# Kernel tuning notes

Measured on AMD Instinct MI355X. Metric: run time of the kernel, lower is better.

## Reference

```python
import jax, jax.numpy as jnp
import numpy as np

DIM = 1024
N_HEADS = 16
HEAD_DIM = DIM // N_HEADS
LN_EPS = 1e-5


def layer_norm(x, gamma, beta, eps=LN_EPS):
    mu = jnp.mean(x, axis=-1, keepdims=True)
    var = jnp.var(x, axis=-1, keepdims=True)
    return (x - mu) * jax.lax.rsqrt(var + eps) * gamma + beta


def setup_inputs() -> dict:
    key = jax.random.key(0)
    ks = jax.random.split(key, 12)
    B, Nq, Nc, D = 2, 1024, 4096, DIM
    s = 1.0 / np.sqrt(D)  # torch Linear default init scale (uniform bound)
    inp = {
        "query": jax.random.normal(ks[0], (B, Nq, D), jnp.float32),
        "context": jax.random.normal(ks[1], (B, Nc, D), jnp.float32),
        "wq": jax.random.uniform(ks[2], (D, D), jnp.float32, -s, s),
        "bq": jax.random.uniform(ks[3], (D,), jnp.float32, -s, s),
        "wk": jax.random.uniform(ks[4], (D, D), jnp.float32, -s, s),
        "bk": jax.random.uniform(ks[5], (D,), jnp.float32, -s, s),
        "wv": jax.random.uniform(ks[6], (D, D), jnp.float32, -s, s),
        "bv": jax.random.uniform(ks[7], (D,), jnp.float32, -s, s),
        "wo": jax.random.uniform(ks[8], (D, D), jnp.float32, -s, s),
        "bo": jax.random.uniform(ks[9], (D,), jnp.float32, -s, s),
        "g_q": jnp.ones((D,), jnp.float32),
        "b_q": jnp.zeros((D,), jnp.float32),
        "g_kv": jnp.ones((D,), jnp.float32),
        "b_kv": jnp.zeros((D,), jnp.float32),
    }
    return inp


def reference(query, context, wq, bq, wk, bk, wv, bv, wo, bo, g_q, b_q, g_kv, b_kv):
    B, Nq, D = query.shape
    Nc = context.shape[1]
    H, Hd = N_HEADS, HEAD_DIM

    qn = layer_norm(query, g_q, b_q)        # [B,Nq,D]
    cn = layer_norm(context, g_kv, b_kv)    # [B,Nc,D]

    # torch Linear: y = x @ W.T + b; weights here stored as [out,in]
    Q = (jnp.einsum('bnd,ed->bne', qn, wq) + bq).reshape(B, Nq, H, Hd)
    K = (jnp.einsum('bnd,ed->bne', cn, wk) + bk).reshape(B, Nc, H, Hd)
    V = (jnp.einsum('bnd,ed->bne', cn, wv) + bv).reshape(B, Nc, H, Hd)

    scale = 1.0 / np.sqrt(Hd)
    scores = jnp.einsum('bqhd,bkhd->bhqk', Q, K) * scale  # [B,H,Nq,Nc]
    attn = jax.nn.softmax(scores, axis=-1)
    out = jnp.einsum('bhqk,bkhd->bqhd', attn, V).reshape(B, Nq, D)

    return qn + (jnp.einsum('bnd,ed->bne', out, wo) + bo)
```

## Files before the change

kernel.cpp:

```cpp
#include <hip/hip_runtime.h>

typedef unsigned short u16;
typedef __attribute__((ext_vector_type(8))) __bf16 bf16x8;
typedef __attribute__((ext_vector_type(4))) float f32x4;

struct alignas(8) U16x4 { u16 x, y, z, w; };

#define MFMA16(a, b, c) __builtin_amdgcn_mfma_f32_16x16x32_bf16(a, b, c, 0, 0, 0)

__device__ __forceinline__ u16 f2bf(float f) {
    union { float f; unsigned u; } v; v.f = f;
    unsigned r = v.u + 0x7fffu + ((v.u >> 16) & 1u);
    return (u16)(r >> 16);
}

__device__ __forceinline__ unsigned cvt_pk_bf16(float lo, float hi) {
    unsigned r;
    asm("v_cvt_pk_bf16_f32 %0, %1, %2" : "=v"(r) : "v"(lo), "v"(hi));
    return r;
}

__device__ __forceinline__ float fexp2(float x) {
    float r;
    asm("v_exp_f32 %0, %1" : "=v"(r) : "v"(x));
    return r;
}

__device__ __forceinline__ void gload_lds16(const void* g, void* l) {
    __builtin_amdgcn_global_load_lds(
        (__attribute__((address_space(1))) void*)g,
        (__attribute__((address_space(3))) void*)l, 16, 0, 0);
}

__global__ __launch_bounds__(256)
void prep(const float* __restrict__ query, const float* __restrict__ context,
          const float* __restrict__ g_q, const float* __restrict__ b_q,
          const float* __restrict__ g_kv, const float* __restrict__ b_kv,
          float* __restrict__ qn32, u16* __restrict__ qnb, u16* __restrict__ cnb,
          const float4* __restrict__ w0, const float4* __restrict__ w1,
          const float4* __restrict__ w2, const float4* __restrict__ w3,
          U16x4* __restrict__ o0, U16x4* __restrict__ o1,
          U16x4* __restrict__ o2, U16x4* __restrict__ o3)
{
    const int blk = blockIdx.x;
    if (blk < 2560) {
        const float *x, *g, *be; float* y32; u16* y16; int rb;
        if (blk < 512) { x = query;   g = g_q;  be = b_q;  y32 = qn32;    y16 = qnb; rb = blk; }
        else           { x = context; g = g_kv; be = b_kv; y32 = nullptr; y16 = cnb; rb = blk - 512; }
        const int wid = threadIdx.x >> 6, lane = threadIdx.x & 63;
        const size_t row = (size_t)rb * 4 + wid;
        const float4* xr = (const float4*)(x + row * 1024);
        float4 v[4];
        float s = 0.f, ss = 0.f;
#pragma unroll
        for (int i = 0; i < 4; ++i) {
            v[i] = xr[i * 64 + lane];
            s  += (v[i].x + v[i].y) + (v[i].z + v[i].w);
            ss += (v[i].x * v[i].x + v[i].y * v[i].y) + (v[i].z * v[i].z + v[i].w * v[i].w);
        }
#pragma unroll
        for (int o = 32; o; o >>= 1) { s += __shfl_xor(s, o, 64); ss += __shfl_xor(ss, o, 64); }
        const float mu = s * (1.f / 1024.f);
        const float rstd = rsqrtf(ss * (1.f / 1024.f) - mu * mu + 1e-5f);
#pragma unroll
        for (int i = 0; i < 4; ++i) {
            float4 gv = ((const float4*)g)[i * 64 + lane];
            float4 bv = ((const float4*)be)[i * 64 + lane];
            float4 o;
            o.x = (v[i].x - mu) * rstd * gv.x + bv.x;
            o.y = (v[i].y - mu) * rstd * gv.y + bv.y;
            o.z = (v[i].z - mu) * rstd * gv.z + bv.z;
            o.w = (v[i].w - mu) * rstd * gv.w + bv.w;
            if (y32) ((float4*)(y32 + row * 1024))[i * 64 + lane] = o;
            U16x4 pk = { f2bf(o.x), f2bf(o.y), f2bf(o.z), f2bf(o.w) };
            ((U16x4*)(y16 + row * 1024))[i * 64 + lane] = pk;
        }
    } else {
        const int i = (blk - 2560) * 256 + threadIdx.x;
        float4 v;
        v = w0[i]; o0[i] = { f2bf(v.x), f2bf(v.y), f2bf(v.z), f2bf(v.w) };
        v = w1[i]; o1[i] = { f2bf(v.x), f2bf(v.y), f2bf(v.z), f2bf(v.w) };
        v = w2[i]; o2[i] = { f2bf(v.x), f2bf(v.y), f2bf(v.z), f2bf(v.w) };
        v = w3[i]; o3[i] = { f2bf(v.x), f2bf(v.y), f2bf(v.z), f2bf(v.w) };
    }
}

__global__ __launch_bounds__(512, 4)
void gemm_kv(const u16* __restrict__ A, const u16* __restrict__ Wk,
             const u16* __restrict__ Wv, const float* __restrict__ bkp,
             const float* __restrict__ bvp, u16* __restrict__ Kout,
             u16* __restrict__ Vt)
{
    constexpr int K = 1024, N = 1024, BK = 64;
    __shared__ __align__(16) u16 sA[128 * BK];
    __shared__ __align__(16) u16 sK[128 * BK];
    __shared__ __align__(16) u16 sV[128 * BK];
    const int tid = threadIdx.x, wid = tid >> 6, lane = tid & 63;
    const int lr = lane & 15, lg = lane >> 4;
    const int wr = wid >> 2, wc = wid & 3;
    const int row0 = blockIdx.x * 128, col0 = blockIdx.y * 128;
    const int srow = wid * 8 + (lane >> 3), scol = (lane & 7) * 8;

    const u16* Ag = A  + (size_t)(row0 + srow) * K + scol;
    const u16* Kg = Wk + (size_t)(col0 + srow) * K + scol;
    const u16* Vg = Wv + (size_t)(col0 + srow) * K + scol;

    f32x4 ka[4][2], va[4][2];
#pragma unroll
    for (int m = 0; m < 4; ++m)
#pragma unroll
        for (int n = 0; n < 2; ++n) {
            ka[m][n] = (f32x4){0.f, 0.f, 0.f, 0.f};
            va[m][n] = (f32x4){0.f, 0.f, 0.f, 0.f};
        }

    for (int k0 = 0; k0 < K; k0 += BK) {
        __syncthreads();
#pragma unroll
        for (int i = 0; i < 2; ++i) {
            gload_lds16(Ag + (size_t)i * 64 * K + k0, (char*)sA + i * 8192 + wid * 1024);
            gload_lds16(Kg + (size_t)i * 64 * K + k0, (char*)sK + i * 8192 + wid * 1024);
            gload_lds16(Vg + (size_t)i * 64 * K + k0, (char*)sV + i * 8192 + wid * 1024);
        }
        __syncthreads();
#pragma unroll
        for (int kk = 0; kk < 2; ++kk) {
            bf16x8 af[4], bk[2], bv[2];
#pragma unroll
            for (int m = 0; m < 4; ++m)
                af[m] = *(const bf16x8*)&sA[(wr * 64 + m * 16 + lr) * BK + kk * 32 + lg * 8];
#pragma unroll
            for (int n = 0; n < 2; ++n) {
                bk[n] = *(const bf16x8*)&sK[(wc * 32 + n * 16 + lr) * BK + kk * 32 + lg * 8];
                bv[n] = *(const bf16x8*)&sV[(wc * 32 + n * 16 + lr) * BK + kk * 32 + lg * 8];
            }
#pragma unroll
            for (int m = 0; m < 4; ++m)
#pragma unroll
                for (int n = 0; n < 2; ++n) {
                    ka[m][n] = MFMA16(af[m], bk[n], ka[m][n]);
                    va[m][n] = MFMA16(af[m], bv[n], va[m][n]);
                }
        }
    }

#pragma unroll
    for (int m = 0; m < 4; ++m) {
#pragma unroll
        for (int n = 0; n < 2; ++n) {
            const int r = row0 + wr * 64 + m * 16 + lg * 4;
            const int c = col0 + wc * 32 + n * 16 + lr;
            const float kb = bkp[c], vb = bvp[c];
#pragma unroll
            for (int j = 0; j < 4; ++j)
                Kout[(size_t)(r + j) * N + c] = f2bf(ka[m][n][j] + kb);
            const size_t base = ((size_t)(r >> 12) * 1024 + c) * 4096 + (r & 4095);
            U16x4 pk = { f2bf(va[m][n][0] + vb), f2bf(va[m][n][1] + vb),
                         f2bf(va[m][n][2] + vb), f2bf(va[m][n][3] + vb) };
            *(U16x4*)&Vt[base] = pk;
        }
    }
}

template<int MODE>
__global__ __launch_bounds__(256)
void gemm_bt64(const u16* __restrict__ A, const u16* __restrict__ W,
               const float* __restrict__ bias, const float* __restrict__ resid,
               void* __restrict__ Cp, int M, int N, int K, float alpha)
{
    constexpr int BK = 64;
    __shared__ __align__(16) u16 sA[64 * BK];
    __shared__ __align__(16) u16 sB[128 * BK];
    const int tid = threadIdx.x, wid = tid >> 6, lane = tid & 63;
    const int lr = lane & 15, lg = lane >> 4;
    const int wr = wid >> 1, wc = wid & 1;
    const int row0 = blockIdx.x * 64, col0 = blockIdx.y * 128;
    const int srow = wid * 8 + (lane >> 3), scol = (lane & 7) * 8;

    const u16* Ag = A + (size_t)(row0 + srow) * K + scol;
    const u16* Wg = W + (size_t)(col0 + srow) * K + scol;

    f32x4 acc[2][4];
#pragma unroll
    for (int m = 0; m < 2; ++m)
#pragma unroll
        for (int n = 0; n < 4; ++n) acc[m][n] = (f32x4){0.f, 0.f, 0.f, 0.f};

    for (int k0 = 0; k0 < K; k0 += BK) {
        __syncthreads();
#pragma unroll
        for (int i = 0; i < 2; ++i)
            gload_lds16(Ag + (size_t)i * 32 * K + k0, (char*)sA + i * 4096 + wid * 1024);
#pragma unroll
        for (int i = 0; i < 4; ++i)
            gload_lds16(Wg + (size_t)i * 32 * K + k0, (char*)sB + i * 4096 + wid * 1024);
        __syncthreads();
#pragma unroll
        for (int kk = 0; kk < 2; ++kk) {
            bf16x8 af[2], bfr[4];
#pragma unroll
            for (int m = 0; m < 2; ++m)
                af[m] = *(const bf16x8*)&sA[(wr * 32 + m * 16 + lr) * BK + kk * 32 + lg * 8];
#pragma unroll
            for (int n = 0; n < 4; ++n)
                bfr[n] = *(const bf16x8*)&sB[(wc * 64 + n * 16 + lr) * BK + kk * 32 + lg * 8];
#pragma unroll
            for (int m = 0; m < 2; ++m)
#pragma unroll
                for (int n = 0; n < 4; ++n)
                    acc[m][n] = MFMA16(af[m], bfr[n], acc[m][n]);
        }
    }

#pragma unroll
    for (int m = 0; m < 2; ++m) {
#pragma unroll
        for (int n = 0; n < 4; ++n) {
            const int r = row0 + wr * 32 + m * 16 + lg * 4;
            const int c = col0 + wc * 64 + n * 16 + lr;
            const float bv = bias[c];
            if constexpr (MODE == 0) {
                u16* C = (u16*)Cp;
#pragma unroll
                for (int j = 0; j < 4; ++j)
                    C[(size_t)(r + j) * N + c] = f2bf((acc[m][n][j] + bv) * alpha);
            } else {
                float* C = (float*)Cp;
#pragma unroll
                for (int j = 0; j < 4; ++j)
                    C[(size_t)(r + j) * N + c] =
                        (acc[m][n][j] + bv) * alpha + resid[(size_t)(r + j) * N + c];
            }
        }
    }
}

__global__ __launch_bounds__(512, 4)
void attn_fwd(const u16* __restrict__ Q, const u16* __restrict__ Kg,
              const u16* __restrict__ Vt, u16* __restrict__ O)
{
    constexpr int D = 1024, CSTR = 19;
    __shared__ __align__(16) char smem[81920];

    const int tid = threadIdx.x, wid = tid >> 6, lane = tid & 63;
    const int grp = wid >> 2, w = wid & 3;
    const int lr = lane & 15, lg = lane >> 4;
    const int rs = lr & 7;
    const int pkey = (lr & 7) << 4;

    const int fid = blockIdx.x;
    const int wkid = (fid & 7) * 64 + (fid >> 3);
    const int qblk = wkid & 15, h = (wkid >> 4) & 15, b = wkid >> 8;
    const int q0 = qblk * 64 + w * 16;

    const u16* Qrow = Q + (size_t)(b * 1024 + q0 + lr) * D + h * 64;
    const bf16x8 qf0 = *(const bf16x8*)(Qrow + lg * 8);
    const bf16x8 qf1 = *(const bf16x8*)(Qrow + 32 + lg * 8);

    const int srow = w * 8 + (lane >> 3);
    const int scol = ((lane & 7) ^ (srow & 7)) * 8;
    const u16* kp = Kg + (size_t)(b * 4096 + grp * 2048 + srow) * D + h * 64 + scol;
    const u16* vp = Vt + ((size_t)(b * 16 + h) * 64 + srow) * 4096 + grp * 2048 + scol;

    char* sProw = smem + 65536 + wid * 2048 + lr * 128;

    f32x4 po[4];
#pragma unroll
    for (int df = 0; df < 4; ++df) po[df] = (f32x4){0.f, 0.f, 0.f, 0.f};
    float m = -INFINITY, l = 0.f;
    bf16x8 vr0, vr1, vr2, vr3, vr4, vr5, vr6, vr7;

    auto pv_step = [&]() {
        bf16x8 pf0 = *(const bf16x8*)(sProw + ((lg * 16) ^ pkey));
        bf16x8 pf1 = *(const bf16x8*)(sProw + ((64 + lg * 16) ^ pkey));
        po[0] = MFMA16(vr0, pf0, po[0]);
        po[1] = MFMA16(vr1, pf0, po[1]);
        po[2] = MFMA16(vr2, pf0, po[2]);
        po[3] = MFMA16(vr3, pf0, po[3]);
        po[0] = MFMA16(vr4, pf1, po[0]);
        po[1] = MFMA16(vr5, pf1, po[1]);
        po[2] = MFMA16(vr6, pf1, po[2]);
        po[3] = MFMA16(vr7, pf1, po[3]);
    };

    {
        char* kd = smem + grp * 8192 + w * 1024;
        char* vd = smem + 32768 + grp * 8192 + w * 1024;
        gload_lds16(kp,                      kd);
        gload_lds16(kp + (size_t)32 * D,     kd + 4096);
        gload_lds16(vp,                      vd);
        gload_lds16(vp + (size_t)32 * 4096,  vd + 4096);
        kp += (size_t)64 * D; vp += 64;
    }
    asm volatile("s_waitcnt vmcnt(0)" ::: "memory");
    asm volatile("s_barrier" ::: "memory");

    for (int t = 0; t < 32; ++t) {
        const int cur = t & 1;
        if (t < 31) {
            char* kd = smem + (cur ^ 1) * 16384 + grp * 8192 + w * 1024;
            char* vd = smem + 32768 + (cur ^ 1) * 16384 + grp * 8192 + w * 1024;
            gload_lds16(kp,                      kd);
            gload_lds16(kp + (size_t)32 * D,     kd + 4096);
            gload_lds16(vp,                      vd);
            gload_lds16(vp + (size_t)32 * 4096,  vd + 4096);
            kp += (size_t)64 * D; vp += 64;
        }

        const u16* kb = (const u16*)(smem + cur * 16384 + grp * 8192);
        const u16* vb = (const u16*)(smem + 32768 + cur * 16384 + grp * 8192);

        __builtin_amdgcn_s_setprio(1);
        if (t > 0) pv_step();

        f32x4 s4[4];
#pragma unroll
        for (int f = 0; f < 4; ++f) {
            const int r = f * 16 + lr;
            bf16x8 k0v = *(const bf16x8*)&kb[r * 64 + (lg ^ rs) * 8];
            bf16x8 k1v = *(const bf16x8*)&kb[r * 64 + ((lg + 4) ^ rs) * 8];
            f32x4 z = (f32x4){0.f, 0.f, 0.f, 0.f};
            z = MFMA16(k0v, qf0, z);
            s4[f] = MFMA16(k1v, qf1, z);
        }
        __builtin_amdgcn_s_setprio(0);

        vr0 = *(const bf16x8*)&vb[(0 * 16 + lr) * 64 + ((0 + lg) ^ rs) * 8];
        vr1 = *(const bf16x8*)&vb[(1 * 16 + lr) * 64 + ((0 + lg) ^ rs) * 8];
        vr2 = *(const bf16x8*)&vb[(2 * 16 + lr) * 64 + ((0 + lg) ^ rs) * 8];
        vr3 = *(const bf16x8*)&vb[(3 * 16 + lr) * 64 + ((0 + lg) ^ rs) * 8];
        vr4 = *(const bf16x8*)&vb[(0 * 16 + lr) * 64 + ((4 + lg) ^ rs) * 8];
        vr5 = *(const bf16x8*)&vb[(1 * 16 + lr) * 64 + ((4 + lg) ^ rs) * 8];
        vr6 = *(const bf16x8*)&vb[(2 * 16 + lr) * 64 + ((4 + lg) ^ rs) * 8];
        vr7 = *(const bf16x8*)&vb[(3 * 16 + lr) * 64 + ((4 + lg) ^ rs) * 8];

        float pmax = fmaxf(fmaxf(fmaxf(s4[0][0], s4[0][1]), fmaxf(s4[0][2], s4[0][3])),
                     fmaxf(fmaxf(fmaxf(s4[1][0], s4[1][1]), fmaxf(s4[1][2], s4[1][3])),
                     fmaxf(fmaxf(fmaxf(s4[2][0], s4[2][1]), fmaxf(s4[2][2], s4[2][3])),
                           fmaxf(fmaxf(s4[3][0], s4[3][1]), fmaxf(s4[3][2], s4[3][3])))));
        if (!__all(pmax <= m)) {
            float tmax = fmaxf(pmax, __shfl_xor(pmax, 16, 64));
            tmax = fmaxf(tmax, __shfl_xor(tmax, 32, 64));
            const float mn = fmaxf(m, tmax);
            const float corr = fexp2(m - mn);
            l *= corr;
#pragma unroll
            for (int df = 0; df < 4; ++df) po[df] *= corr;
            m = mn;
        }
        float lsum = 0.f;
        uint2 pk[4];
#pragma unroll
        for (int f = 0; f < 4; ++f) {
            float p0 = fexp2(s4[f][0] - m);
            float p1 = fexp2(s4[f][1] - m);
            float p2 = fexp2(s4[f][2] - m);
            float p3 = fexp2(s4[f][3] - m);
            lsum += (p0 + p1) + (p2 + p3);
            pk[f].x = cvt_pk_bf16(p0, p1);
            pk[f].y = cvt_pk_bf16(p2, p3);
        }
        l += lsum;

#pragma unroll
        for (int f = 0; f < 4; ++f)
            *(uint2*)(sProw + ((f * 32 + lg * 8) ^ pkey)) = pk[f];

        asm volatile("s_waitcnt vmcnt(0) lgkmcnt(0)" ::: "memory");
        asm volatile("s_barrier" ::: "memory");
    }

    pv_step();

    l += __shfl_xor(l, 16, 64);
    l += __shfl_xor(l, 32, 64);

    float* cb = (float*)smem;
    if (grp == 1) {
        float* dst = cb + (size_t)(w * 64 + lane) * CSTR;
        dst[0] = m; dst[1] = l;
#pragma unroll
        for (int df = 0; df < 4; ++df)
#pragma unroll
            for (int j = 0; j < 4; ++j) dst[2 + df * 4 + j] = po[df][j];
    }
    __syncthreads();
    if (grp == 0) {
        const float* src = cb + (size_t)(w * 64 + lane) * CSTR;
        const float m1 = src[0], l1 = src[1];
        const float M = fmaxf(m, m1);
        const float c0 = fexp2(m - M), c1 = fexp2(m1 - M);
        const float rl = 1.f / (l * c0 + l1 * c1);
        u16* Orow = O + (size_t)(b * 1024 + q0 + lr) * D + h * 64;
#pragma unroll
        for (int df = 0; df < 4; ++df) {
            U16x4 opk = { f2bf((po[df][0] * c0 + src[2 + df * 4 + 0] * c1) * rl),
                          f2bf((po[df][1] * c0 + src[2 + df * 4 + 1] * c1) * rl),
                          f2bf((po[df][2] * c0 + src[2 + df * 4 + 2] * c1) * rl),
                          f2bf((po[df][3] * c0 + src[2 + df * 4 + 3] * c1) * rl) };
            *(U16x4*)&Orow[df * 16 + lg * 4] = opk;
        }
    }
}

extern "C" void kernel_launch(void* const* d_in, const int* in_sizes, int n_in,
                              void* d_out, int out_size, void* d_ws, size_t ws_size,
                              hipStream_t stream)
{
    const float* query   = (const float*)d_in[0];
    const float* context = (const float*)d_in[1];
    const float* wq = (const float*)d_in[2];
    const float* bq = (const float*)d_in[3];
    const float* wk = (const float*)d_in[4];
    const float* bk = (const float*)d_in[5];
    const float* wv = (const float*)d_in[6];
    const float* bv = (const float*)d_in[7];
    const float* wo = (const float*)d_in[8];
    const float* bo = (const float*)d_in[9];
    const float* g_q  = (const float*)d_in[10];
    const float* b_q  = (const float*)d_in[11];
    const float* g_kv = (const float*)d_in[12];
    const float* b_kv = (const float*)d_in[13];

    char* p = (char*)d_ws;
    auto alloc = [&](size_t bytes) { char* r = p; p += (bytes + 255) & ~(size_t)255; return r; };
    u16*   wqb  = (u16*)alloc(1024 * 1024 * 2);
    u16*   wkb  = (u16*)alloc(1024 * 1024 * 2);
    u16*   wvb  = (u16*)alloc(1024 * 1024 * 2);
    u16*   wob  = (u16*)alloc(1024 * 1024 * 2);
    float* qn32 = (float*)alloc((size_t)2048 * 1024 * 4);
    u16*   qnb  = (u16*)alloc((size_t)2048 * 1024 * 2);
    u16*   cnb  = (u16*)alloc((size_t)8192 * 1024 * 2);
    u16*   Qb   = (u16*)alloc((size_t)2048 * 1024 * 2);
    u16*   Kb   = (u16*)alloc((size_t)8192 * 1024 * 2);
    u16*   Vtb  = (u16*)alloc((size_t)8192 * 1024 * 2);
    u16*   AOb  = (u16*)alloc((size_t)2048 * 1024 * 2);

    prep<<<3584, 256, 0, stream>>>(query, context, g_q, b_q, g_kv, b_kv,
                                   qn32, qnb, cnb,
                                   (const float4*)wq, (const float4*)wk,
                                   (const float4*)wv, (const float4*)wo,
                                   (U16x4*)wqb, (U16x4*)wkb, (U16x4*)wvb, (U16x4*)wob);

    gemm_bt64<0><<<dim3(32, 8), 256, 0, stream>>>(qnb, wqb, bq, nullptr, Qb, 2048, 1024, 1024, 0.18033688f);
    gemm_kv<<<dim3(64, 8), 512, 0, stream>>>(cnb, wkb, wvb, bk, bv, Kb, Vtb);

    attn_fwd<<<dim3(512), 512, 0, stream>>>(Qb, Kb, Vtb, AOb);

    gemm_bt64<1><<<dim3(32, 8), 256, 0, stream>>>(AOb, wob, bo, qn32, d_out, 2048, 1024, 1024, 1.0f);
}
```

Measured before the change: 164.6 us.

## Merge Q projection into KV GEMM launch, stage V transpose through LDS, simplify attention PV

Folds the Q projection GEMM into the K/V projection kernel as one 640-block launch with an XCD-aware block remap, removing a launch and letting the small Q work fill the tail. The V output is now transposed through shared memory and written as coalesced 16-byte rows instead of scattered 8-byte stores. The attention kernel drops its software-pipelined PV step, priority hints and preloaded V registers, and does the PV MFMAs inline after writing P. This cuts register pressure but loses the overlap of PV with the next QK.

```diff
diff --git a/kernel.cpp b/kernel.cpp
--- a/kernel.cpp
+++ b/kernel.cpp
@@ -3,6 +3,7 @@
 typedef unsigned short u16;
 typedef __attribute__((ext_vector_type(8))) __bf16 bf16x8;
 typedef __attribute__((ext_vector_type(4))) float f32x4;
+typedef __attribute__((ext_vector_type(4))) unsigned U32x4;
 
 struct alignas(8) U16x4 { u16 x, y, z, w; };
 
@@ -86,87 +87,162 @@
 }
 
 __global__ __launch_bounds__(512, 4)
-void gemm_kv(const u16* __restrict__ A, const u16* __restrict__ Wk,
-             const u16* __restrict__ Wv, const float* __restrict__ bkp,
-             const float* __restrict__ bvp, u16* __restrict__ Kout,
-             u16* __restrict__ Vt)
+void qkv_gemm(const u16* __restrict__ cnb, const u16* __restrict__ qnb,
+              const u16* __restrict__ Wk, const u16* __restrict__ Wv,
+              const u16* __restrict__ Wq, const float* __restrict__ bkp,
+              const float* __restrict__ bvp, const float* __restrict__ bqp,
+              u16* __restrict__ Kout, u16* __restrict__ Vt, u16* __restrict__ Qout,
+              float alpha)
 {
     constexpr int K = 1024, N = 1024, BK = 64;
-    __shared__ __align__(16) u16 sA[128 * BK];
-    __shared__ __align__(16) u16 sK[128 * BK];
-    __shared__ __align__(16) u16 sV[128 * BK];
+    __shared__ __align__(16) char smem[49152];
+    u16* sA = (u16*)smem;
+    u16* sB = (u16*)(smem + 16384);
+    u16* sC = (u16*)(smem + 32768);
+
     const int tid = threadIdx.x, wid = tid >> 6, lane = tid & 63;
     const int lr = lane & 15, lg = lane >> 4;
     const int wr = wid >> 2, wc = wid & 3;
-    const int row0 = blockIdx.x * 128, col0 = blockIdx.y * 128;
     const int srow = wid * 8 + (lane >> 3), scol = (lane & 7) * 8;
 
-    const u16* Ag = A  + (size_t)(row0 + srow) * K + scol;
-    const u16* Kg = Wk + (size_t)(col0 + srow) * K + scol;
-    const u16* Vg = Wv + (size_t)(col0 + srow) * K + scol;
-
-    f32x4 ka[4][2], va[4][2];
-#pragma unroll
-    for (int m = 0; m < 4; ++m)
-#pragma unroll
-        for (int n = 0; n < 2; ++n) {
-            ka[m][n] = (f32x4){0.f, 0.f, 0.f, 0.f};
-            va[m][n] = (f32x4){0.f, 0.f, 0.f, 0.f};
-        }
-
-    for (int k0 = 0; k0 < K; k0 += BK) {
+    const int fid = blockIdx.x;
+    const int w = (fid & 7) * 80 + (fid >> 3);
+    const bool is_kv = (w < 512);
+
+    if (is_kv) {
+        const int row0 = (w >> 3) * 128, col0 = (w & 7) * 128;
+        const u16* Ag = cnb + (size_t)(row0 + srow) * K + scol;
+        const u16* Kg = Wk  + (size_t)(col0 + srow) * K + scol;
+        const u16* Vg = Wv  + (size_t)(col0 + srow) * K + scol;
+
+        f32x4 ka[4][2], va[4][2];
+#pragma unroll
+        for (int m = 0; m < 4; ++m)
+#pragma unroll
+            for (int n = 0; n < 2; ++n) {
+                ka[m][n] = (f32x4){0.f, 0.f, 0.f, 0.f};
+                va[m][n] = (f32x4){0.f, 0.f, 0.f, 0.f};
+            }
+
+        for (int k0 = 0; k0 < K; k0 += BK) {
+            __syncthreads();
+#pragma unroll
+            for (int i = 0; i < 2; ++i) {
+                gload_lds16(Ag + (size_t)i * 64 * K + k0, (char*)sA + i * 8192 + wid * 1024);
+                gload_lds16(Kg + (size_t)i * 64 * K + k0, (char*)sB + i * 8192 + wid * 1024);
+                gload_lds16(Vg + (size_t)i * 64 * K + k0, (char*)sC + i * 8192 + wid * 1024);
+            }
+            __syncthreads();
+#pragma unroll
+            for (int kk = 0; kk < 2; ++kk) {
+                bf16x8 af[4], bk[2], bv[2];
+#pragma unroll
+                for (int m = 0; m < 4; ++m)
+                    af[m] = *(const bf16x8*)&sA[(wr * 64 + m * 16 + lr) * BK + kk * 32 + lg * 8];
+#pragma unroll
+                for (int n = 0; n < 2; ++n) {
+                    bk[n] = *(const bf16x8*)&sB[(wc * 32 + n * 16 + lr) * BK + kk * 32 + lg * 8];
+                    bv[n] = *(const bf16x8*)&sC[(wc * 32 + n * 16 + lr) * BK + kk * 32 + lg * 8];
+                }
+#pragma unroll
+                for (int m = 0; m < 4; ++m)
+#pragma unroll
+                    for (int n = 0; n < 2; ++n) {
+                        ka[m][n] = MFMA16(af[m], bk[n], ka[m][n]);
+                        va[m][n] = MFMA16(af[m], bv[n], va[m][n]);
+                    }
+            }
+        }
+
+#pragma unroll
+        for (int m = 0; m < 4; ++m)
+#pragma unroll
+            for (int n = 0; n < 2; ++n) {
+                const int r = row0 + wr * 64 + m * 16 + lg * 4;
+                const int c = col0 + wc * 32 + n * 16 + lr;
+                const float kb = bkp[c];
+#pragma unroll
+                for (int j = 0; j < 4; ++j)
+                    Kout[(size_t)(r + j) * N + c] = f2bf(ka[m][n][j] + kb);
+            }
+
         __syncthreads();
-#pragma unroll
-        for (int i = 0; i < 2; ++i) {
-            gload_lds16(Ag + (size_t)i * 64 * K + k0, (char*)sA + i * 8192 + wid * 1024);
-            gload_lds16(Kg + (size_t)i * 64 * K + k0, (char*)sK + i * 8192 + wid * 1024);
-            gload_lds16(Vg + (size_t)i * 64 * K + k0, (char*)sV + i * 8192 + wid * 1024);
-        }
+        u16* tb = (u16*)smem;
+#pragma unroll
+        for (int m = 0; m < 4; ++m)
+#pragma unroll
+            for (int n = 0; n < 2; ++n) {
+                const int cl = wc * 32 + n * 16 + lr;
+                const int rl = wr * 64 + m * 16 + lg * 4;
+                const float vb = bvp[col0 + cl];
+                U16x4 pk = { f2bf(va[m][n][0] + vb), f2bf(va[m][n][1] + vb),
+                             f2bf(va[m][n][2] + vb), f2bf(va[m][n][3] + vb) };
+                *(U16x4*)&tb[cl * 136 + rl] = pk;
+            }
         __syncthreads();
-#pragma unroll
-        for (int kk = 0; kk < 2; ++kk) {
-            bf16x8 af[4], bk[2], bv[2];
-#pragma unroll
-            for (int m = 0; m < 4; ++m)
-                af[m] = *(const bf16x8*)&sA[(wr * 64 + m * 16 + lr) * BK + kk * 32 + lg * 8];
+        const int bb = row0 >> 12, inner = row0 & 4095;
+        const int chunk = tid & 15;
+#pragma unroll
+        for (int i = 0; i < 4; ++i) {
+            const int c = i * 32 + (tid >> 4);
+            U32x4 v = *(const U32x4*)&tb[c * 136 + chunk * 8];
+            *(U32x4*)&Vt[(size_t)(bb * 1024 + col0 + c) * 4096 + inner + chunk * 8] = v;
+        }
+    } else {
+        const int qi = w - 512;
+        const int row0 = (qi >> 3) * 128, col0 = (qi & 7) * 128;
+        const u16* Ag = qnb + (size_t)(row0 + srow) * K + scol;
+        const u16* Qg = Wq  + (size_t)(col0 + srow) * K + scol;
+
+        f32x4 qa[4][2];
+#pragma unroll
+        for (int m = 0; m < 4; ++m)
+#pragma unroll
+            for (int n = 0; n < 2; ++n) qa[m][n] = (f32x4){0.f, 0.f, 0.f, 0.f};
+
+        for (int k0 = 0; k0 < K; k0 += BK) {
+            __syncthreads();
+#pragma unroll
+            for (int i = 0; i < 2; ++i) {
+                gload_lds16(Ag + (size_t)i * 64 * K + k0, (char*)sA + i * 8192 + wid * 1024);
+                gload_lds16(Qg + (size_t)i * 64 * K + k0, (char*)sB + i * 8192 + wid * 1024);
+            }
+            __syncthreads();
+#pragma unroll
+            for (int kk = 0; kk < 2; ++kk) {
+                bf16x8 af[4], bq[2];
+#pragma unroll
+                for (int m = 0; m < 4; ++m)
+                    af[m] = *(const bf16x8*)&sA[(wr * 64 + m * 16 + lr) * BK + kk * 32 + lg * 8];
+#pragma unroll
+                for (int n = 0; n < 2; ++n)
+                    bq[n] = *(const bf16x8*)&sB[(wc * 32 + n * 16 + lr) * BK + kk * 32 + lg * 8];
+#pragma unroll
+                for (int m = 0; m < 4; ++m)
+#pragma unroll
+                    for (int n = 0; n < 2; ++n)
+                        qa[m][n] = MFMA16(af[m], bq[n], qa[m][n]);
+            }
+        }
+
+#pragma unroll
+        for (int m = 0; m < 4; ++m)
 #pragma unroll
             for (int n = 0; n < 2; ++n) {
-                bk[n] = *(const bf16x8*)&sK[(wc * 32 + n * 16 + lr) * BK + kk * 32 + lg * 8];
-                bv[n] = *(const bf16x8*)&sV[(wc * 32 + n * 16 + lr) * BK + kk * 32 + lg * 8];
-            }
-#pragma unroll
-            for (int m = 0; m < 4; ++m)
-#pragma unroll
-                for (int n = 0; n < 2; ++n) {
-                    ka[m][n] = MFMA16(af[m], bk[n], ka[m][n]);
-                    va[m][n] = MFMA16(af[m], bv[n], va[m][n]);
-                }
-        }
-    }
-
-#pragma unroll
-    for (int m = 0; m < 4; ++m) {
-#pragma unroll
-        for (int n = 0; n < 2; ++n) {
-            const int r = row0 + wr * 64 + m * 16 + lg * 4;
-            const int c = col0 + wc * 32 + n * 16 + lr;
-            const float kb = bkp[c], vb = bvp[c];
-#pragma unroll
-            for (int j = 0; j < 4; ++j)
-                Kout[(size_t)(r + j) * N + c] = f2bf(ka[m][n][j] + kb);
-            const size_t base = ((size_t)(r >> 12) * 1024 + c) * 4096 + (r & 4095);
-            U16x4 pk = { f2bf(va[m][n][0] + vb), f2bf(va[m][n][1] + vb),
-                         f2bf(va[m][n][2] + vb), f2bf(va[m][n][3] + vb) };
-            *(U16x4*)&Vt[base] = pk;
-        }
-    }
-}
-
-template<int MODE>
+                const int r = row0 + wr * 64 + m * 16 + lg * 4;
+                const int c = col0 + wc * 32 + n * 16 + lr;
+                const float bv = bqp[c];
+#pragma unroll
+                for (int j = 0; j < 4; ++j)
+                    Qout[(size_t)(r + j) * N + c] = f2bf((qa[m][n][j] + bv) * alpha);
+            }
+    }
+}
+
 __global__ __launch_bounds__(256)
-void gemm_bt64(const u16* __restrict__ A, const u16* __restrict__ W,
-               const float* __restrict__ bias, const float* __restrict__ resid,
-               void* __restrict__ Cp, int M, int N, int K, float alpha)
+void gemm_o(const u16* __restrict__ A, const u16* __restrict__ W,
+            const float* __restrict__ bias, const float* __restrict__ resid,
+            float* __restrict__ Cp, int M, int N, int K)
 {
     constexpr int BK = 64;
     __shared__ __align__(16) u16 sA[64 * BK];
@@ -213,26 +289,17 @@
     }
 
 #pragma unroll
-    for (int m = 0; m < 2; ++m) {
+    for (int m = 0; m < 2; ++m)
 #pragma unroll
         for (int n = 0; n < 4; ++n) {
             const int r = row0 + wr * 32 + m * 16 + lg * 4;
             const int c = col0 + wc * 64 + n * 16 + lr;
             const float bv = bias[c];
-            if constexpr (MODE == 0) {
-                u16* C = (u16*)Cp;
-#pragma unroll
-                for (int j = 0; j < 4; ++j)
-                    C[(size_t)(r + j) * N + c] = f2bf((acc[m][n][j] + bv) * alpha);
-            } else {
-                float* C = (float*)Cp;
-#pragma unroll
-                for (int j = 0; j < 4; ++j)
-                    C[(size_t)(r + j) * N + c] =
-                        (acc[m][n][j] + bv) * alpha + resid[(size_t)(r + j) * N + c];
-            }
-        }
-    }
+#pragma unroll
+            for (int j = 0; j < 4; ++j)
+                Cp[(size_t)(r + j) * N + c] =
+                    (acc[m][n][j] + bv) + resid[(size_t)(r + j) * N + c];
+        }
 }
 
 __global__ __launch_bounds__(512, 4)
@@ -249,8 +316,8 @@
     const int pkey = (lr & 7) << 4;
 
     const int fid = blockIdx.x;
-    const int wkid = (fid & 7) * 64 + (fid >> 3);
-    const int qblk = wkid & 15, h = (wkid >> 4) & 15, b = wkid >> 8;
+    const int wk = (fid & 7) * 64 + (fid >> 3);
+    const int qblk = wk & 15, h = (wk >> 4) & 15, b = wk >> 8;
     const int q0 = qblk * 64 + w * 16;
 
     const u16* Qrow = Q + (size_t)(b * 1024 + q0 + lr) * D + h * 64;
@@ -268,20 +335,6 @@
 #pragma unroll
     for (int df = 0; df < 4; ++df) po[df] = (f32x4){0.f, 0.f, 0.f, 0.f};
     float m = -INFINITY, l = 0.f;
-    bf16x8 vr0, vr1, vr2, vr3, vr4, vr5, vr6, vr7;
-
-    auto pv_step = [&]() {
-        bf16x8 pf0 = *(const bf16x8*)(sProw + ((lg * 16) ^ pkey));
-        bf16x8 pf1 = *(const bf16x8*)(sProw + ((64 + lg * 16) ^ pkey));
-        po[0] = MFMA16(vr0, pf0, po[0]);
-        po[1] = MFMA16(vr1, pf0, po[1]);
-        po[2] = MFMA16(vr2, pf0, po[2]);
-        po[3] = MFMA16(vr3, pf0, po[3]);
-        po[0] = MFMA16(vr4, pf1, po[0]);
-        po[1] = MFMA16(vr5, pf1, po[1]);
-        po[2] = MFMA16(vr6, pf1, po[2]);
-        po[3] = MFMA16(vr7, pf1, po[3]);
-    };
 
     {
         char* kd = smem + grp * 8192 + w * 1024;
@@ -310,9 +363,6 @@
         const u16* kb = (const u16*)(smem + cur * 16384 + grp * 8192);
         const u16* vb = (const u16*)(smem + 32768 + cur * 16384 + grp * 8192);
 
-        __builtin_amdgcn_s_setprio(1);
-        if (t > 0) pv_step();
-
         f32x4 s4[4];
 #pragma unroll
         for (int f = 0; f < 4; ++f) {
@@ -323,16 +373,6 @@
             z = MFMA16(k0v, qf0, z);
             s4[f] = MFMA16(k1v, qf1, z);
         }
-        __builtin_amdgcn_s_setprio(0);
-
-        vr0 = *(const bf16x8*)&vb[(0 * 16 + lr) * 64 + ((0 + lg) ^ rs) * 8];
-        vr1 = *(const bf16x8*)&vb[(1 * 16 + lr) * 64 + ((0 + lg) ^ rs) * 8];
-        vr2 = *(const bf16x8*)&vb[(2 * 16 + lr) * 64 + ((0 + lg) ^ rs) * 8];
-        vr3 = *(const bf16x8*)&vb[(3 * 16 + lr) * 64 + ((0 + lg) ^ rs) * 8];
-        vr4 = *(const bf16x8*)&vb[(0 * 16 + lr) * 64 + ((4 + lg) ^ rs) * 8];
-        vr5 = *(const bf16x8*)&vb[(1 * 16 + lr) * 64 + ((4 + lg) ^ rs) * 8];
-        vr6 = *(const bf16x8*)&vb[(2 * 16 + lr) * 64 + ((4 + lg) ^ rs) * 8];
-        vr7 = *(const bf16x8*)&vb[(3 * 16 + lr) * 64 + ((4 + lg) ^ rs) * 8];
 
         float pmax = fmaxf(fmaxf(fmaxf(s4[0][0], s4[0][1]), fmaxf(s4[0][2], s4[0][3])),
                      fmaxf(fmaxf(fmaxf(s4[1][0], s4[1][1]), fmaxf(s4[1][2], s4[1][3])),
@@ -366,11 +406,20 @@
         for (int f = 0; f < 4; ++f)
             *(uint2*)(sProw + ((f * 32 + lg * 8) ^ pkey)) = pk[f];
 
-        asm volatile("s_waitcnt vmcnt(0) lgkmcnt(0)" ::: "memory");
+#pragma unroll
+        for (int c = 0; c < 2; ++c) {
+            bf16x8 pf = *(const bf16x8*)(sProw + ((c * 64 + lg * 16) ^ pkey));
+#pragma unroll
+            for (int df = 0; df < 4; ++df) {
+                const int r = df * 16 + lr;
+                bf16x8 vf = *(const bf16x8*)&vb[r * 64 + ((c * 4 + lg) ^ rs) * 8];
+                po[df] = MFMA16(vf, pf, po[df]);
+            }
+        }
+
+        asm volatile("s_waitcnt vmcnt(0)" ::: "memory");
         asm volatile("s_barrier" ::: "memory");
     }
-
-    pv_step();
 
     l += __shfl_xor(l, 16, 64);
     l += __shfl_xor(l, 32, 64);
@@ -442,10 +491,10 @@
                                    (const float4*)wv, (const float4*)wo,
                                    (U16x4*)wqb, (U16x4*)wkb, (U16x4*)wvb, (U16x4*)wob);
 
-    gemm_bt64<0><<<dim3(32, 8), 256, 0, stream>>>(qnb, wqb, bq, nullptr, Qb, 2048, 1024, 1024, 0.18033688f);
-    gemm_kv<<<dim3(64, 8), 512, 0, stream>>>(cnb, wkb, wvb, bk, bv, Kb, Vtb);
+    qkv_gemm<<<dim3(640), 512, 0, stream>>>(cnb, qnb, wkb, wvb, wqb,
+                                            bk, bv, bq, Kb, Vtb, Qb, 0.18033688f);
 
     attn_fwd<<<dim3(512), 512, 0, stream>>>(Qb, Kb, Vtb, AOb);
 
-    gemm_bt64<1><<<dim3(32, 8), 256, 0, stream>>>(AOb, wob, bo, qn32, d_out, 2048, 1024, 1024, 1.0f);
-}
+    gemm_o<<<dim3(32, 8), 256, 0, stream>>>(AOb, wob, bo, qn32, (float*)d_out, 2048, 1024, 1024);
+}
```

New measurement: 174.5 us. 1.06x slower.
